# Performance work log

Measured on AMD Instinct MI355X. Metric: run time of the kernel, lower is better.

Reference implementation:

```python
import jax, jax.numpy as jnp
import numpy as np
import math

EMB = 512
HID = 512
SEQ = 128
BATCH = 64
VOCAB = 10000
NUM_LAYERS = 2


def setup_inputs() -> dict:
    key = jax.random.key(0)
    ks = jax.random.split(key, 16)
    inputs = jax.random.randint(ks[0], (SEQ, BATCH), 0, VOCAB)
    hidden = jnp.zeros((NUM_LAYERS, BATCH, HID), dtype=jnp.float32)
    emb_table = jax.random.normal(ks[1], (VOCAB, EMB), dtype=jnp.float32) * 0.02

    def lin(k, fan_in, fan_out):
        bound = 1.0 / math.sqrt(fan_in)
        kw, kb = jax.random.split(k)
        W = jax.random.uniform(kw, (fan_in, fan_out), minval=-bound, maxval=bound, dtype=jnp.float32)
        b = jax.random.uniform(kb, (fan_out,), minval=-bound, maxval=bound, dtype=jnp.float32)
        return W, b

    # layer 0: input_size = emb + hid; layer 1: input_size = 2*hid
    Wg0, bg0 = lin(ks[2], EMB + HID, 2 * HID)
    Wc0, bc0 = lin(ks[3], EMB + HID, HID)
    Wg1, bg1 = lin(ks[4], 2 * HID, 2 * HID)
    Wc1, bc1 = lin(ks[5], 2 * HID, HID)
    Wout, bout = lin(ks[6], HID, VOCAB)
    return {
        "inputs": inputs, "hidden": hidden, "emb_table": emb_table,
        "Wg0": Wg0, "bg0": bg0, "Wc0": Wc0, "bc0": bc0,
        "Wg1": Wg1, "bg1": bg1, "Wc1": Wc1, "bc1": bc1,
        "Wout": Wout, "bout": bout,
    }


def _gru_forward(inputs, hidden, emb_table, layer_params, Wout, bout):
    # embeddings: [S, B, E], scaled like WordEmbedding
    emb = emb_table[inputs] * jnp.asarray(math.sqrt(EMB), emb_table.dtype)

    def step(h, x_t):
        layer_in = x_t
        new_h = []
        for n, (Wg, bg, Wc, bc) in enumerate(layer_params):
            g = jax.nn.sigmoid(jnp.concatenate([layer_in, h[n]], axis=1) @ Wg + bg)
            update = g[:, :HID]
            reset = g[:, HID:]
            cell = jnp.tanh(jnp.concatenate([layer_in, reset * h[n]], axis=1) @ Wc + bc)
            h_out = (1.0 - update) * h[n] + update * cell
            new_h.append(h_out)
            layer_in = h_out
        logits_t = layer_in @ Wout + bout  # [B, V]
        return jnp.stack(new_h, axis=0), logits_t

    hidden_final, logits = jax.lax.scan(step, hidden, emb)
    return logits, hidden_final  # [S, B, V], [L, B, H]


def reference(inputs, hidden, emb_table, Wg0, bg0, Wc0, bc0, Wg1, bg1, Wc1, bc1, Wout, bout):
    layer_params = [(Wg0, bg0, Wc0, bc0), (Wg1, bg1, Wc1, bc1)]
    return _gru_forward(inputs, hidden, emb_table, layer_params, Wout, bout)
```

## Files before the change

### kernel.cpp

```cpp
#include <hip/hip_runtime.h>
#include <cstdint>
#include <cstddef>

#define SEQ 128
#define BATCH 64
#define EMBD 512
#define HIDD 512
#define NVOCAB 10000
#define NREC 64
#define NWORK 192
#define NTOT 256

typedef __attribute__((ext_vector_type(8))) short short8;
typedef __attribute__((ext_vector_type(4))) float f32x4;

__device__ __forceinline__ unsigned short f2b(float f) {
  union { float f; unsigned u; } c; c.f = f;
  unsigned u = c.u;
  unsigned r = (u + 0x7fffu + ((u >> 16) & 1u)) >> 16;
  return (unsigned short)r;
}

__device__ __forceinline__ f32x4 mfma16(short8 a, short8 b, f32x4 c) {
  return __builtin_amdgcn_mfma_f32_16x16x32_bf16(a, b, c, 0, 0, 0);
}

__device__ __forceinline__ short8 ldg_coh(const unsigned short* p) {
  short8 r;
  asm volatile("global_load_dwordx4 %0, %1, off sc0 sc1" : "=v"(r) : "v"(p));
  return r;
}
__device__ __forceinline__ void stg_coh(unsigned short* p, short8 v) {
  asm volatile("global_store_dwordx4 %0, %1, off sc0 sc1" :: "v"(p), "v"(v) : "memory");
}
__device__ __forceinline__ void st_stamp(int* p, int v) {
  asm volatile("global_store_dword %0, %1, off sc0 sc1" :: "v"(p), "v"(v) : "memory");
}
__device__ __forceinline__ int ld_stamp(const int* p) {
  int r;
  asm volatile("global_load_dword %0, %1, off sc0 sc1" : "=v"(r) : "v"(p));
  return r;
}

template<int SLP>
__device__ __forceinline__ void wait_all32(const int* rep, int need) {
  if (need < 0) return;
  int idx = threadIdx.x & 31;
  int guard = 0;
  for (;;) {
    int v = ld_stamp(rep + idx);
    asm volatile("s_waitcnt vmcnt(0)" ::: "memory");
    if (__all(v >= need)) return;
    __builtin_amdgcn_s_sleep(SLP);
    if (++guard > 3000000) return;
  }
}

__global__ void pack_frag(const float* __restrict__ src, unsigned short* __restrict__ dst,
                          int ksteps, int row_off, int src_ld, int ntiles, int mode, int nreal) {
  int tid = blockIdx.x * 256 + threadIdx.x;
  int total = ntiles * ksteps * 64;
  if (tid >= total) return;
  int l = tid & 63;
  int ks = (tid >> 6) % ksteps;
  int nt = tid / (64 * ksteps);
  int n = nt * 16 + (l & 15);
  int col;
  bool valid = true;
  if (mode == 1) {
    int jc = n >> 5, s = n & 31;
    col = (s < 16) ? (16 * jc + s) : (512 + 16 * jc + (s - 16));
  } else {
    col = n;
    valid = (n < nreal);
  }
  int k0 = row_off + ks * 32 + ((l >> 4) << 3);
  short8 o;
  for (int j = 0; j < 8; ++j) {
    float x = valid ? src[(size_t)(k0 + j) * src_ld + col] : 0.f;
    o[j] = (short)f2b(x);
  }
  *reinterpret_cast<short8*>(&dst[(size_t)tid * 8]) = o;
}

__global__ void pack_bias(const float* __restrict__ bg0, const float* __restrict__ bg1,
                          float* __restrict__ bg0p, float* __restrict__ bg1p) {
  int p = blockIdx.x * 256 + threadIdx.x;
  if (p >= 1024) return;
  int jc = p >> 5, s = p & 31;
  int col = (s < 16) ? (16 * jc + s) : (512 + 16 * jc + (s - 16));
  bg0p[p] = bg0[col];
  bg1p[p] = bg1[col];
}

__global__ void embed_gather(const int* __restrict__ inp, const float* __restrict__ tab,
                             unsigned short* __restrict__ XA) {
  int tid = blockIdx.x * 256 + threadIdx.x;
  if (tid >= SEQ * 64 * 64) return;
  int row = tid & 63;
  int kt = (tid >> 6) & 63;
  int t = tid >> 12;
  int v = inp[t * BATCH + row];
  const float* s = &tab[(size_t)v * EMBD + kt * 8];
  const float scale = 22.627416997969522f;
  short8 o;
  for (int j = 0; j < 8; ++j) o[j] = (short)f2b(s[j] * scale);
  *reinterpret_cast<short8*>(&XA[(size_t)tid * 8]) = o;
}

__global__ void init_states(const float* __restrict__ hid, unsigned short* __restrict__ H0B1,
                            unsigned short* __restrict__ H1INITB, int* __restrict__ stamps) {
  int idx = blockIdx.x * 256 + threadIdx.x;
  if (idx < 24 * 64) stamps[idx] = -1;
  if (idx >= 64 * 512) return;
  int row = idx >> 9, c = idx & 511;
  size_t ko = (((size_t)(c >> 3)) * 64 + row) * 8 + (c & 7);
  H0B1[ko] = f2b(hid[idx]);
  H1INITB[ko] = f2b(hid[64 * 512 + idx]);
}

__launch_bounds__(256, 2)
__global__ void gemm128(const unsigned short* __restrict__ A, const unsigned short* __restrict__ Bf,
                        const float* __restrict__ bias, float* __restrict__ C,
                        int Nld, int Nreal) {
  __shared__ __align__(16) unsigned short ldsA[16 * 512];
  __shared__ __align__(16) unsigned short ldsB[16 * 512];
  int nb = blockIdx.x, yb = blockIdx.y;
  int l = threadIdx.x & 63, w = threadIdx.x >> 6;
  int mh = w >> 1, nh = w & 1;
  f32x4 acc[4][4] = {};
  for (int ko = 0; ko < 8; ++ko) {
    __syncthreads();
    for (int j = 0; j < 4; ++j) {
      int c = w * 4 + j;
      int m8 = c >> 1, ks = c & 1;
      int t = yb * 2 + (m8 >> 2);
      int kt = ko * 8 + ks * 4 + (l >> 4);
      int row = (m8 & 3) * 16 + (l & 15);
      size_t gidx = (((size_t)t * 64 + kt) * 64 + row) * 8;
      *reinterpret_cast<short8*>(&ldsA[(size_t)c * 512 + l * 8]) =
          *reinterpret_cast<const short8*>(&A[gidx]);
      size_t gb = (((size_t)(nb * 8 + (c >> 1)) * 16) + (size_t)(ko * 2 + (c & 1))) * 512 + (size_t)l * 8;
      *reinterpret_cast<short8*>(&ldsB[(size_t)c * 512 + l * 8]) =
          *reinterpret_cast<const short8*>(&Bf[gb]);
    }
    __syncthreads();
    for (int ks = 0; ks < 2; ++ks) {
      short8 a[4], b[4];
      for (int mt = 0; mt < 4; ++mt) {
        int m8 = mh * 4 + mt;
        a[mt] = *reinterpret_cast<const short8*>(&ldsA[((size_t)(m8 * 2 + ks) * 64 + l) * 8]);
      }
      for (int nt = 0; nt < 4; ++nt) {
        int n8 = nh * 4 + nt;
        b[nt] = *reinterpret_cast<const short8*>(&ldsB[((size_t)(n8 * 2 + ks) * 64 + l) * 8]);
      }
      for (int mt = 0; mt < 4; ++mt)
        for (int nt = 0; nt < 4; ++nt)
          acc[mt][nt] = mfma16(a[mt], b[nt], acc[mt][nt]);
    }
  }
  for (int mt = 0; mt < 4; ++mt) {
    for (int nt = 0; nt < 4; ++nt) {
      int col = nb * 128 + nh * 64 + nt * 16 + (l & 15);
      if (col >= Nreal) continue;
      float bv = bias[col];
      int row0 = yb * 128 + mh * 64 + mt * 16 + ((l >> 4) << 2);
      for (int r = 0; r < 4; ++r)
        C[(size_t)(row0 + r) * Nld + col] = acc[mt][nt][r] + bv;
    }
  }
}

template<int KS, int LAYER>
__device__ void rec_layer(
    int g, const unsigned short* __restrict__ Wg, const unsigned short* __restrict__ Wc,
    const float* __restrict__ Xg0p, const float* __restrict__ Xc0p,
    const float* __restrict__ bg1p, const float* __restrict__ bc1,
    const float* __restrict__ hidden,
    unsigned short* __restrict__ H0Bx, unsigned short* __restrict__ H1ALL,
    const unsigned short* __restrict__ H1INITB,
    unsigned short* __restrict__ RH0, unsigned short* __restrict__ RH1,
    int* __restrict__ stamps, float* __restrict__ hidden_out, char* smem) {
  constexpr int KQ = KS / 4;
  constexpr int NH = KQ / 4;
  float (*red)[64][33] = (float(*)[64][33])smem;
  float (*u_lds)[17] = (float(*)[17])(smem + 33792);
  float (*hf)[17] = (float(*)[17])(smem + 38144);
  const int tid = threadIdx.x;
  const int l = tid & 63, w = tid >> 6;
  const int s = l & 15, q = l >> 4;

  int* SR   = stamps + (LAYER ? 4 : 0) * 64;
  int* SH0  = stamps + 8 * 64;
  int* SH1  = stamps + 12 * 64;
  int* SHW  = stamps + 16 * 64;
  int* mySH = LAYER ? SH1 : SH0;
  const int repw = ((g + w) & 3) * 64;
  unsigned short* myRH = LAYER ? RH1 : RH0;

  short8 bg[2][KQ];
  short8 bc[KQ];
#pragma unroll
  for (int kk = 0; kk < KQ; ++kk) {
    int ks = w * KQ + kk;
    bg[0][kk] = *reinterpret_cast<const short8*>(&Wg[(((size_t)(2 * g) * KS + ks) * 64 + l) * 8]);
    bg[1][kk] = *reinterpret_cast<const short8*>(&Wg[(((size_t)(2 * g + 1) * KS + ks) * 64 + l) * 8]);
    bc[kk]    = *reinterpret_cast<const short8*>(&Wc[(((size_t)g * KS + ks) * 64 + l) * 8]);
  }

  {
    int col = tid & 15;
#pragma unroll
    for (int rr = 0; rr < 4; ++rr) {
      int row = (tid >> 4) * 4 + rr;
      hf[row][col] = hidden[(size_t)LAYER * 32768 + (size_t)row * 512 + 16 * g + col];
    }
  }
  __syncthreads();

  for (int t = 0; t < 128; ++t) {
    const unsigned short* h0b = H0Bx + (size_t)32768 * (LAYER ? (t & 1) : ((t + 1) & 1));

    wait_all32<2>(SH0 + repw, LAYER ? t : t - 1);
    if (LAYER) wait_all32<2>(SH1 + repw, t - 1);
    const unsigned short* hi = h0b;
    if (LAYER) hi = (t >= 1) ? (H1ALL + (size_t)(t - 1) * 32768) : H1INITB;
    {
      f32x4 acc[4][2] = {};
#pragma unroll
      for (int hb = 0; hb < NH; ++hb) {
        short8 a[4][4];
#pragma unroll
        for (int kk2 = 0; kk2 < 4; ++kk2) {
          int ks = w * KQ + hb * 4 + kk2;
          const unsigned short* ab = (KS == 32 && ks >= 16) ? hi : h0b;
          int kl = ks & 15;
#pragma unroll
          for (int mt = 0; mt < 4; ++mt)
            a[kk2][mt] = ldg_coh(&ab[(((size_t)(kl * 4 + q)) * 64 + mt * 16 + s) * 8]);
        }
        asm volatile("s_waitcnt vmcnt(0)" ::: "memory");
        __builtin_amdgcn_sched_barrier(0);
#pragma unroll
        for (int kk2 = 0; kk2 < 4; ++kk2)
#pragma unroll
          for (int mt = 0; mt < 4; ++mt) {
            acc[mt][0] = mfma16(a[kk2][mt], bg[0][hb * 4 + kk2], acc[mt][0]);
            acc[mt][1] = mfma16(a[kk2][mt], bg[1][hb * 4 + kk2], acc[mt][1]);
          }
      }
#pragma unroll
      for (int mt = 0; mt < 4; ++mt)
#pragma unroll
        for (int nt = 0; nt < 2; ++nt)
#pragma unroll
          for (int r = 0; r < 4; ++r)
            red[w][mt * 16 + q * 4 + r][nt * 16 + s] = acc[mt][nt][r];
    }
    __syncthreads();
    if (tid < 128) {
      int row = tid & 63, kg = tid >> 6;
      short8 o;
#pragma unroll
      for (int j = 0; j < 8; ++j) {
        int col = 16 + kg * 8 + j;
        float sum = red[0][row][col] + red[1][row][col] + red[2][row][col] + red[3][row][col];
        sum += LAYER ? bg1p[g * 32 + col]
                     : Xg0p[((size_t)(t * 64 + row)) * 1024 + g * 32 + col];
        float gate = 1.f / (1.f + __expf(-sum));
        o[j] = (short)f2b(gate * hf[row][kg * 8 + j]);
      }
      stg_coh(&myRH[((size_t)(2 * g + kg) * 64 + row) * 8], o);
    } else {
      int t2 = tid - 128;
      int row = t2 & 63, kg = t2 >> 6;
#pragma unroll
      for (int j = 0; j < 8; ++j) {
        int col = kg * 8 + j;
        float sum = red[0][row][col] + red[1][row][col] + red[2][row][col] + red[3][row][col];
        sum += LAYER ? bg1p[g * 32 + col]
                     : Xg0p[((size_t)(t * 64 + row)) * 1024 + g * 32 + col];
        u_lds[row][col] = 1.f / (1.f + __expf(-sum));
      }
    }
    asm volatile("s_waitcnt vmcnt(0)" ::: "memory");
    __syncthreads();
    if (tid == 0) {
#pragma unroll
      for (int r = 0; r < 4; ++r) st_stamp(&SR[r * 64 + g], t);
    }

    wait_all32<2>(SR + repw, t);
    {
      f32x4 acc[4] = {};
#pragma unroll
      for (int hb = 0; hb < NH; ++hb) {
        short8 a[4][4];
#pragma unroll
        for (int kk2 = 0; kk2 < 4; ++kk2) {
          int ks = w * KQ + hb * 4 + kk2;
          const unsigned short* ab = (KS == 32 && ks < 16) ? h0b : myRH;
          int kl = ks & 15;
#pragma unroll
          for (int mt = 0; mt < 4; ++mt)
            a[kk2][mt] = ldg_coh(&ab[(((size_t)(kl * 4 + q)) * 64 + mt * 16 + s) * 8]);
        }
        asm volatile("s_waitcnt vmcnt(0)" ::: "memory");
        __builtin_amdgcn_sched_barrier(0);
#pragma unroll
        for (int kk2 = 0; kk2 < 4; ++kk2)
#pragma unroll
          for (int mt = 0; mt < 4; ++mt)
            acc[mt] = mfma16(a[kk2][mt], bc[hb * 4 + kk2], acc[mt]);
      }
#pragma unroll
      for (int mt = 0; mt < 4; ++mt)
#pragma unroll
        for (int r = 0; r < 4; ++r)
          red[w][mt * 16 + q * 4 + r][s] = acc[mt][r];
    }
    __syncthreads();
    if (tid < 128) {
      int row = tid & 63, kg = tid >> 6;
      short8 o;
#pragma unroll
      for (int j = 0; j < 8; ++j) {
        int cl = kg * 8 + j;
        float sum = red[0][row][cl] + red[1][row][cl] + red[2][row][cl] + red[3][row][cl];
        sum += LAYER ? bc1[16 * g + cl]
                     : Xc0p[((size_t)(t * 64 + row)) * 512 + 16 * g + cl];
        float cv = tanhf(sum);
        float u = u_lds[row][cl];
        float hp = hf[row][cl];
        float hn = hp + u * (cv - hp);
        hf[row][cl] = hn;
        o[j] = (short)f2b(hn);
      }
      if (LAYER == 0) stg_coh(&H0Bx[((size_t)(t & 1)) * 32768 + ((size_t)(2 * g + kg) * 64 + row) * 8], o);
      else            stg_coh(&H1ALL[(size_t)t * 32768 + ((size_t)(2 * g + kg) * 64 + row) * 8], o);
    }
    asm volatile("s_waitcnt vmcnt(0)" ::: "memory");
    __syncthreads();
    if (tid == 0) {
#pragma unroll
      for (int r = 0; r < 4; ++r) st_stamp(&mySH[r * 64 + g], t);
      if (LAYER) {
#pragma unroll
        for (int r = 0; r < 8; ++r) st_stamp(&SHW[r * 64 + g], t);
      }
    }
  }

  {
    int col = tid & 15;
#pragma unroll
    for (int rr = 0; rr < 4; ++rr) {
      int row = (tid >> 4) * 4 + rr;
      hidden_out[(size_t)LAYER * 32768 + (size_t)row * 512 + 16 * g + col] = hf[row][col];
    }
  }
}

__device__ void worker_path(int wid, const unsigned short* __restrict__ A,
                            const unsigned short* __restrict__ Bf,
                            const float* __restrict__ bias, float* __restrict__ C,
                            const int* __restrict__ stamps, char* smem) {
  unsigned short* ldsA = (unsigned short*)smem;
  unsigned short* ldsB = (unsigned short*)(smem + 16384);
  const int* rep = stamps + (16 + (wid & 7)) * 64;
  int l = threadIdx.x & 63, w = threadIdx.x >> 6;
  int mh = w >> 1, nh = w & 1;
  for (int id = wid; id < 64 * 80; id += NWORK) {
    int tp = id / 80, nb = id - tp * 80;
    wait_all32<16>(rep, 2 * tp + 1);
    f32x4 acc[4][4] = {};
    for (int ko = 0; ko < 8; ++ko) {
      __syncthreads();
      for (int j = 0; j < 4; ++j) {
        int c = w * 4 + j;
        int m8 = c >> 1, ks = c & 1;
        int t = tp * 2 + (m8 >> 2);
        int kt = ko * 8 + ks * 4 + (l >> 4);
        int row = (m8 & 3) * 16 + (l & 15);
        size_t gidx = (((size_t)t * 64 + kt) * 64 + row) * 8;
        *reinterpret_cast<short8*>(&ldsA[(size_t)c * 512 + l * 8]) =
            *reinterpret_cast<const short8*>(&A[gidx]);
        size_t gb = (((size_t)(nb * 8 + (c >> 1)) * 16) + (size_t)(ko * 2 + (c & 1))) * 512 + (size_t)l * 8;
        *reinterpret_cast<short8*>(&ldsB[(size_t)c * 512 + l * 8]) =
            *reinterpret_cast<const short8*>(&Bf[gb]);
      }
      __syncthreads();
      for (int ks = 0; ks < 2; ++ks) {
        short8 a[4], b[4];
        for (int mt = 0; mt < 4; ++mt)
          a[mt] = *reinterpret_cast<const short8*>(&ldsA[((size_t)((mh * 4 + mt) * 2 + ks) * 64 + l) * 8]);
        for (int nt = 0; nt < 4; ++nt)
          b[nt] = *reinterpret_cast<const short8*>(&ldsB[((size_t)((nh * 4 + nt) * 2 + ks) * 64 + l) * 8]);
        for (int mt = 0; mt < 4; ++mt)
          for (int nt = 0; nt < 4; ++nt)
            acc[mt][nt] = mfma16(a[mt], b[nt], acc[mt][nt]);
      }
    }
    for (int mt = 0; mt < 4; ++mt) {
      for (int nt = 0; nt < 4; ++nt) {
        int col = nb * 128 + nh * 64 + nt * 16 + (l & 15);
        if (col >= NVOCAB) continue;
        float bv = bias[col];
        int row0 = tp * 128 + mh * 64 + mt * 16 + ((l >> 4) << 2);
        for (int r = 0; r < 4; ++r)
          C[(size_t)(row0 + r) * NVOCAB + col] = acc[mt][nt][r] + bv;
      }
    }
  }
}

__launch_bounds__(256, 1)
__global__ void fused_persist(const unsigned short* __restrict__ Wg0h, const unsigned short* __restrict__ Wc0h,
                              const unsigned short* __restrict__ Wg1, const unsigned short* __restrict__ Wc1,
                              const float* __restrict__ Xg0p, const float* __restrict__ Xc0p,
                              const float* __restrict__ bg1p, const float* __restrict__ bc1,
                              const float* __restrict__ hidden,
                              unsigned short* __restrict__ H0Bx, unsigned short* __restrict__ H1ALL,
                              const unsigned short* __restrict__ H1INITB,
                              unsigned short* __restrict__ RH0, unsigned short* __restrict__ RH1,
                              int* __restrict__ stamps, float* __restrict__ hidden_out,
                              const unsigned short* __restrict__ Wout_f, const float* __restrict__ bout,
                              float* __restrict__ out) {
  __shared__ __align__(16) char smem[42496];
  int wg = blockIdx.x;
  if (wg >= NREC) {
    worker_path(wg - NREC, H1ALL, Wout_f, bout, out, stamps, smem);
    return;
  }
  int g = wg & 31;
  if (wg < 32)
    rec_layer<16, 0>(g, Wg0h, Wc0h, Xg0p, Xc0p, bg1p, bc1, hidden, H0Bx, H1ALL,
                     H1INITB, RH0, RH1, stamps, hidden_out, smem);
  else
    rec_layer<32, 1>(g, Wg1, Wc1, Xg0p, Xc0p, bg1p, bc1, hidden, H0Bx, H1ALL,
                     H1INITB, RH0, RH1, stamps, hidden_out, smem);
}

static inline int gridFor(long long n) { return (int)((n + 255) / 256); }

extern "C" void kernel_launch(void* const* d_in, const int* in_sizes, int n_in,
                              void* d_out, int out_size, void* d_ws, size_t ws_size,
                              hipStream_t stream) {
  const int*   inputs = (const int*)d_in[0];
  const float* hidden = (const float*)d_in[1];
  const float* embtab = (const float*)d_in[2];
  const float* Wg0 = (const float*)d_in[3];
  const float* bg0 = (const float*)d_in[4];
  const float* Wc0 = (const float*)d_in[5];
  const float* bc0 = (const float*)d_in[6];
  const float* Wg1 = (const float*)d_in[7];
  const float* bg1 = (const float*)d_in[8];
  const float* Wc1 = (const float*)d_in[9];
  const float* bc1 = (const float*)d_in[10];
  const float* Wout = (const float*)d_in[11];
  const float* bout = (const float*)d_in[12];
  float* out = (float*)d_out;

  char* p = (char*)d_ws;
  size_t off = 0;
  auto carve = [&](size_t bytes) { char* r = p + off; off += (bytes + 255) & ~(size_t)255; return (void*)r; };
  unsigned short* XA     = (unsigned short*)carve((size_t)8192 * 512 * 2);
  unsigned short* Wg0x_f = (unsigned short*)carve((size_t)512 * 1024 * 2);
  unsigned short* Wg0h_f = (unsigned short*)carve((size_t)512 * 1024 * 2);
  unsigned short* Wc0x_f = (unsigned short*)carve((size_t)512 * 512 * 2);
  unsigned short* Wc0h_f = (unsigned short*)carve((size_t)512 * 512 * 2);
  unsigned short* Wg1_f  = (unsigned short*)carve((size_t)1024 * 1024 * 2);
  unsigned short* Wc1_f  = (unsigned short*)carve((size_t)1024 * 512 * 2);
  unsigned short* Wout_f = (unsigned short*)carve((size_t)512 * 10240 * 2);
  float* Xg0p = (float*)carve((size_t)8192 * 1024 * 4);
  float* Xc0p = (float*)carve((size_t)8192 * 512 * 4);
  unsigned short* H1ALL  = (unsigned short*)carve((size_t)128 * 32768 * 2);
  unsigned short* H0Bx   = (unsigned short*)carve((size_t)2 * 32768 * 2);
  unsigned short* H1INITB= (unsigned short*)carve((size_t)32768 * 2);
  unsigned short* RH0 = (unsigned short*)carve((size_t)32768 * 2);
  unsigned short* RH1 = (unsigned short*)carve((size_t)32768 * 2);
  float* bg0p = (float*)carve(1024 * 4);
  float* bg1p = (float*)carve(1024 * 4);
  int* stamps = (int*)carve(24 * 64 * 4);
  if (off > ws_size) return;

  pack_frag<<<gridFor(64LL * 16 * 64), 256, 0, stream>>>(Wg0, Wg0x_f, 16, 0,   1024, 64, 1, 1024);
  pack_frag<<<gridFor(64LL * 16 * 64), 256, 0, stream>>>(Wg0, Wg0h_f, 16, 512, 1024, 64, 1, 1024);
  pack_frag<<<gridFor(32LL * 16 * 64), 256, 0, stream>>>(Wc0, Wc0x_f, 16, 0,   512,  32, 0, 512);
  pack_frag<<<gridFor(32LL * 16 * 64), 256, 0, stream>>>(Wc0, Wc0h_f, 16, 512, 512,  32, 0, 512);
  pack_frag<<<gridFor(64LL * 32 * 64), 256, 0, stream>>>(Wg1, Wg1_f,  32, 0,   1024, 64, 1, 1024);
  pack_frag<<<gridFor(32LL * 32 * 64), 256, 0, stream>>>(Wc1, Wc1_f,  32, 0,   512,  32, 0, 512);
  pack_frag<<<gridFor(640LL * 16 * 64), 256, 0, stream>>>(Wout, Wout_f, 16, 0, 10000, 640, 0, 10000);
  pack_bias<<<4, 256, 0, stream>>>(bg0, bg1, bg0p, bg1p);

  embed_gather<<<gridFor((long long)SEQ * 64 * 64), 256, 0, stream>>>(inputs, embtab, XA);
  init_states<<<gridFor(32768), 256, 0, stream>>>(hidden, H0Bx + 32768, H1INITB, stamps);

  gemm128<<<dim3(8, 64), 256, 0, stream>>>(XA, Wg0x_f, bg0p, Xg0p, 1024, 1024);
  gemm128<<<dim3(4, 64), 256, 0, stream>>>(XA, Wc0x_f, bc0, Xc0p, 512, 512);

  fused_persist<<<NTOT, 256, 0, stream>>>(Wg0h_f, Wc0h_f, Wg1_f, Wc1_f, Xg0p, Xc0p,
                                          bg1p, bc1, hidden, H0Bx, H1ALL, H1INITB,
                                          RH0, RH1, stamps, out + (size_t)81920000,
                                          Wout_f, bout, out);
}
```

Baseline: 1.376 ms.

## Give each timestep its own hidden-state buffer and use ordinary cached loads

```diff
diff --git a/kernel.cpp b/kernel.cpp
--- a/kernel.cpp
+++ b/kernel.cpp
@@ -4,8 +4,6 @@
 
 #define SEQ 128
 #define BATCH 64
-#define EMBD 512
-#define HIDD 512
 #define NVOCAB 10000
 #define NREC 64
 #define NWORK 192
@@ -25,11 +23,6 @@
   return __builtin_amdgcn_mfma_f32_16x16x32_bf16(a, b, c, 0, 0, 0);
 }
 
-__device__ __forceinline__ short8 ldg_coh(const unsigned short* p) {
-  short8 r;
-  asm volatile("global_load_dwordx4 %0, %1, off sc0 sc1" : "=v"(r) : "v"(p));
-  return r;
-}
 __device__ __forceinline__ void stg_coh(unsigned short* p, short8 v) {
   asm volatile("global_store_dwordx4 %0, %1, off sc0 sc1" :: "v"(p), "v"(v) : "memory");
 }
@@ -101,21 +94,21 @@
   int kt = (tid >> 6) & 63;
   int t = tid >> 12;
   int v = inp[t * BATCH + row];
-  const float* s = &tab[(size_t)v * EMBD + kt * 8];
+  const float* s = &tab[(size_t)v * 512 + kt * 8];
   const float scale = 22.627416997969522f;
   short8 o;
   for (int j = 0; j < 8; ++j) o[j] = (short)f2b(s[j] * scale);
   *reinterpret_cast<short8*>(&XA[(size_t)tid * 8]) = o;
 }
 
-__global__ void init_states(const float* __restrict__ hid, unsigned short* __restrict__ H0B1,
+__global__ void init_states(const float* __restrict__ hid, unsigned short* __restrict__ H0INITB,
                             unsigned short* __restrict__ H1INITB, int* __restrict__ stamps) {
   int idx = blockIdx.x * 256 + threadIdx.x;
   if (idx < 24 * 64) stamps[idx] = -1;
   if (idx >= 64 * 512) return;
   int row = idx >> 9, c = idx & 511;
   size_t ko = (((size_t)(c >> 3)) * 64 + row) * 8 + (c & 7);
-  H0B1[ko] = f2b(hid[idx]);
+  H0INITB[ko] = f2b(hid[idx]);
   H1INITB[ko] = f2b(hid[64 * 512 + idx]);
 }
 
@@ -178,15 +171,13 @@
     const float* __restrict__ Xg0p, const float* __restrict__ Xc0p,
     const float* __restrict__ bg1p, const float* __restrict__ bc1,
     const float* __restrict__ hidden,
-    unsigned short* __restrict__ H0Bx, unsigned short* __restrict__ H1ALL,
-    const unsigned short* __restrict__ H1INITB,
-    unsigned short* __restrict__ RH0, unsigned short* __restrict__ RH1,
-    int* __restrict__ stamps, float* __restrict__ hidden_out, char* smem) {
+    unsigned short* __restrict__ H0ALL, unsigned short* __restrict__ H1ALL,
+    const unsigned short* __restrict__ H0INITB, const unsigned short* __restrict__ H1INITB,
+    unsigned short* __restrict__ RH0ALL, unsigned short* __restrict__ RH1ALL,
+    int* __restrict__ stamps, float* __restrict__ hidden_out,
+    float (&red)[4][64][33], float (&u_lds)[64][17], float (&hf)[64][17]) {
   constexpr int KQ = KS / 4;
   constexpr int NH = KQ / 4;
-  float (*red)[64][33] = (float(*)[64][33])smem;
-  float (*u_lds)[17] = (float(*)[17])(smem + 33792);
-  float (*hf)[17] = (float(*)[17])(smem + 38144);
   const int tid = threadIdx.x;
   const int l = tid & 63, w = tid >> 6;
   const int s = l & 15, q = l >> 4;
@@ -197,7 +188,6 @@
   int* SHW  = stamps + 16 * 64;
   int* mySH = LAYER ? SH1 : SH0;
   const int repw = ((g + w) & 3) * 64;
-  unsigned short* myRH = LAYER ? RH1 : RH0;
 
   short8 bg[2][KQ];
   short8 bc[KQ];
@@ -220,12 +210,17 @@
   __syncthreads();
 
   for (int t = 0; t < 128; ++t) {
-    const unsigned short* h0b = H0Bx + (size_t)32768 * (LAYER ? (t & 1) : ((t + 1) & 1));
-
-    wait_all32<2>(SH0 + repw, LAYER ? t : t - 1);
-    if (LAYER) wait_all32<2>(SH1 + repw, t - 1);
-    const unsigned short* hi = h0b;
-    if (LAYER) hi = (t >= 1) ? (H1ALL + (size_t)(t - 1) * 32768) : H1INITB;
+    if constexpr (LAYER == 0) {
+      wait_all32<2>(SH0 + repw, t - 1);
+    } else {
+      wait_all32<2>(SH0 + repw, t);
+      wait_all32<2>(SH1 + repw, t - 1);
+    }
+    const unsigned short* A0 = LAYER ? (H0ALL + (size_t)t * 32768)
+                                     : (t ? (H0ALL + (size_t)(t - 1) * 32768) : H0INITB);
+    const unsigned short* A1 = nullptr;
+    if (LAYER) A1 = t ? (H1ALL + (size_t)(t - 1) * 32768) : H1INITB;
+    unsigned short* myRH = (LAYER ? RH1ALL : RH0ALL) + (size_t)t * 32768;
     {
       f32x4 acc[4][2] = {};
 #pragma unroll
@@ -234,14 +229,12 @@
 #pragma unroll
         for (int kk2 = 0; kk2 < 4; ++kk2) {
           int ks = w * KQ + hb * 4 + kk2;
-          const unsigned short* ab = (KS == 32 && ks >= 16) ? hi : h0b;
+          const unsigned short* ab = (KS == 32 && ks >= 16) ? A1 : A0;
           int kl = ks & 15;
 #pragma unroll
           for (int mt = 0; mt < 4; ++mt)
-            a[kk2][mt] = ldg_coh(&ab[(((size_t)(kl * 4 + q)) * 64 + mt * 16 + s) * 8]);
+            a[kk2][mt] = *reinterpret_cast<const short8*>(&ab[(((size_t)(kl * 4 + q)) * 64 + mt * 16 + s) * 8]);
         }
-        asm volatile("s_waitcnt vmcnt(0)" ::: "memory");
-        __builtin_amdgcn_sched_barrier(0);
 #pragma unroll
         for (int kk2 = 0; kk2 < 4; ++kk2)
 #pragma unroll
@@ -300,14 +293,12 @@
 #pragma unroll
         for (int kk2 = 0; kk2 < 4; ++kk2) {
           int ks = w * KQ + hb * 4 + kk2;
-          const unsigned short* ab = (KS == 32 && ks < 16) ? h0b : myRH;
+          const unsigned short* ab = (KS == 32 && ks < 16) ? A0 : myRH;
           int kl = ks & 15;
 #pragma unroll
           for (int mt = 0; mt < 4; ++mt)
-            a[kk2][mt] = ldg_coh(&ab[(((size_t)(kl * 4 + q)) * 64 + mt * 16 + s) * 8]);
+            a[kk2][mt] = *reinterpret_cast<const short8*>(&ab[(((size_t)(kl * 4 + q)) * 64 + mt * 16 + s) * 8]);
         }
-        asm volatile("s_waitcnt vmcnt(0)" ::: "memory");
-        __builtin_amdgcn_sched_barrier(0);
 #pragma unroll
         for (int kk2 = 0; kk2 < 4; ++kk2)
 #pragma unroll
@@ -337,8 +328,9 @@
         hf[row][cl] = hn;
         o[j] = (short)f2b(hn);
       }
-      if (LAYER == 0) stg_coh(&H0Bx[((size_t)(t & 1)) * 32768 + ((size_t)(2 * g + kg) * 64 + row) * 8], o);
-      else            stg_coh(&H1ALL[(size_t)t * 32768 + ((size_t)(2 * g + kg) * 64 + row) * 8], o);
+      size_t ko = ((size_t)(2 * g + kg) * 64 + row) * 8;
+      if (LAYER == 0) stg_coh(&H0ALL[(size_t)t * 32768 + ko], o);
+      else            stg_coh(&H1ALL[(size_t)t * 32768 + ko], o);
     }
     asm volatile("s_waitcnt vmcnt(0)" ::: "memory");
     __syncthreads();
@@ -421,9 +413,9 @@
                               const float* __restrict__ Xg0p, const float* __restrict__ Xc0p,
                               const float* __restrict__ bg1p, const float* __restrict__ bc1,
                               const float* __restrict__ hidden,
-                              unsigned short* __restrict__ H0Bx, unsigned short* __restrict__ H1ALL,
-                              const unsigned short* __restrict__ H1INITB,
-                              unsigned short* __restrict__ RH0, unsigned short* __restrict__ RH1,
+                              unsigned short* __restrict__ H0ALL, unsigned short* __restrict__ H1ALL,
+                              const unsigned short* __restrict__ H0INITB, const unsigned short* __restrict__ H1INITB,
+                              unsigned short* __restrict__ RH0ALL, unsigned short* __restrict__ RH1ALL,
                               int* __restrict__ stamps, float* __restrict__ hidden_out,
                               const unsigned short* __restrict__ Wout_f, const float* __restrict__ bout,
                               float* __restrict__ out) {
@@ -433,13 +425,18 @@
     worker_path(wg - NREC, H1ALL, Wout_f, bout, out, stamps, smem);
     return;
   }
+  float (*red)[64][33] = (float(*)[64][33])smem;
+  float (*u_lds)[17] = (float(*)[17])(smem + 33792);
+  float (*hf)[17] = (float(*)[17])(smem + 38144);
   int g = wg & 31;
   if (wg < 32)
-    rec_layer<16, 0>(g, Wg0h, Wc0h, Xg0p, Xc0p, bg1p, bc1, hidden, H0Bx, H1ALL,
-                     H1INITB, RH0, RH1, stamps, hidden_out, smem);
+    rec_layer<16, 0>(g, Wg0h, Wc0h, Xg0p, Xc0p, bg1p, bc1, hidden, H0ALL, H1ALL,
+                     H0INITB, H1INITB, RH0ALL, RH1ALL, stamps, hidden_out,
+                     *(float(*)[4][64][33])red, *(float(*)[64][17])u_lds, *(float(*)[64][17])hf);
   else
-    rec_layer<32, 1>(g, Wg1, Wc1, Xg0p, Xc0p, bg1p, bc1, hidden, H0Bx, H1ALL,
-                     H1INITB, RH0, RH1, stamps, hidden_out, smem);
+    rec_layer<32, 1>(g, Wg1, Wc1, Xg0p, Xc0p, bg1p, bc1, hidden, H0ALL, H1ALL,
+                     H0INITB, H1INITB, RH0ALL, RH1ALL, stamps, hidden_out,
+                     *(float(*)[4][64][33])red, *(float(*)[64][17])u_lds, *(float(*)[64][17])hf);
 }
 
 static inline int gridFor(long long n) { return (int)((n + 255) / 256); }
@@ -476,10 +473,11 @@
   float* Xg0p = (float*)carve((size_t)8192 * 1024 * 4);
   float* Xc0p = (float*)carve((size_t)8192 * 512 * 4);
   unsigned short* H1ALL  = (unsigned short*)carve((size_t)128 * 32768 * 2);
-  unsigned short* H0Bx   = (unsigned short*)carve((size_t)2 * 32768 * 2);
+  unsigned short* H0ALL  = (unsigned short*)carve((size_t)128 * 32768 * 2);
+  unsigned short* RH0ALL = (unsigned short*)carve((size_t)128 * 32768 * 2);
+  unsigned short* RH1ALL = (unsigned short*)carve((size_t)128 * 32768 * 2);
+  unsigned short* H0INITB= (unsigned short*)carve((size_t)32768 * 2);
   unsigned short* H1INITB= (unsigned short*)carve((size_t)32768 * 2);
-  unsigned short* RH0 = (unsigned short*)carve((size_t)32768 * 2);
-  unsigned short* RH1 = (unsigned short*)carve((size_t)32768 * 2);
   float* bg0p = (float*)carve(1024 * 4);
   float* bg1p = (float*)carve(1024 * 4);
   int* stamps = (int*)carve(24 * 64 * 4);
@@ -495,13 +493,14 @@
   pack_bias<<<4, 256, 0, stream>>>(bg0, bg1, bg0p, bg1p);
 
   embed_gather<<<gridFor((long long)SEQ * 64 * 64), 256, 0, stream>>>(inputs, embtab, XA);
-  init_states<<<gridFor(32768), 256, 0, stream>>>(hidden, H0Bx + 32768, H1INITB, stamps);
+  init_states<<<gridFor(32768), 256, 0, stream>>>(hidden, H0INITB, H1INITB, stamps);
 
   gemm128<<<dim3(8, 64), 256, 0, stream>>>(XA, Wg0x_f, bg0p, Xg0p, 1024, 1024);
   gemm128<<<dim3(4, 64), 256, 0, stream>>>(XA, Wc0x_f, bc0, Xc0p, 512, 512);
 
   fused_persist<<<NTOT, 256, 0, stream>>>(Wg0h_f, Wc0h_f, Wg1_f, Wc1_f, Xg0p, Xc0p,
-                                          bg1p, bc1, hidden, H0Bx, H1ALL, H1INITB,
-                                          RH0, RH1, stamps, out + (size_t)81920000,
+                                          bg1p, bc1, hidden, H0ALL, H1ALL,
+                                          H0INITB, H1INITB, RH0ALL, RH1ALL,
+                                          stamps, out + (size_t)81920000,
                                           Wout_f, bout, out);
 }
```

After: 1.736 ms. +26.1%, slower.
